# Kernel optimization log

Hardware: AMD Instinct MI355X
Metric: run time of the kernel (lower is better)

The kernel has to match this reference:

```python
import jax, jax.numpy as jnp
import numpy as np

EMBED_DIM = 1024
NUM_HEADS = 16
HEAD_DIM = EMBED_DIM // NUM_HEADS


def setup_inputs() -> dict:
    key = jax.random.key(0)
    ks = jax.random.split(key, 9)
    B, S, D = 2, 2048, EMBED_DIM
    scale = 1.0 / np.sqrt(D)
    x = jax.random.normal(ks[0], (B, S, D), dtype=jnp.float32)
    Wq = jax.random.normal(ks[1], (D, D), dtype=jnp.float32) * scale
    Wk = jax.random.normal(ks[2], (D, D), dtype=jnp.float32) * scale
    Wv = jax.random.normal(ks[3], (D, D), dtype=jnp.float32) * scale
    Wo = jax.random.normal(ks[4], (D, D), dtype=jnp.float32) * scale
    bq = jnp.zeros((D,), jnp.float32)
    bk = jnp.zeros((D,), jnp.float32)
    bv = jnp.zeros((D,), jnp.float32)
    bo = jnp.zeros((D,), jnp.float32)
    return {"x": x, "Wq": Wq, "bq": bq, "Wk": Wk, "bk": bk,
            "Wv": Wv, "bv": bv, "Wo": Wo, "bo": bo}


def reference(x, Wq, bq, Wk, bk, Wv, bv, Wo, bo):
    B, S, D = x.shape
    H, Dh = NUM_HEADS, HEAD_DIM
    # QKV projections -> [B, H, S, Dh]
    q = (x @ Wq + bq).reshape(B, S, H, Dh).transpose(0, 2, 1, 3)
    k = (x @ Wk + bk).reshape(B, S, H, Dh).transpose(0, 2, 1, 3)
    v = (x @ Wv + bv).reshape(B, S, H, Dh).transpose(0, 2, 1, 3)
    # scores [B, H, S, S], scaled by sqrt(head_dim)
    scores = jnp.einsum('bhqd,bhkd->bhqk', q, k) / jnp.sqrt(jnp.float32(Dh))
    attn = jax.nn.softmax(scores, axis=-1)
    out = jnp.einsum('bhqk,bhkd->bhqd', attn, v)  # [B, H, S, Dh]
    out = out.transpose(0, 2, 1, 3).reshape(B, S, D)
    return out @ Wo + bo
```

## Files before the change

kernel.cpp:

```cpp
#include <hip/hip_runtime.h>
#include <hip/hip_bf16.h>

typedef short bf16x8 __attribute__((ext_vector_type(8)));
typedef float f32x4 __attribute__((ext_vector_type(4)));
typedef unsigned uint2v __attribute__((ext_vector_type(2)));

#define MFMA16(a, b, c) __builtin_amdgcn_mfma_f32_16x16x32_bf16((a), (b), (c), 0, 0, 0)

#if __has_builtin(__builtin_amdgcn_exp2f)
#define EXP2(x) __builtin_amdgcn_exp2f(x)
#else
#define EXP2(x) exp2f(x)
#endif

static constexpr int B_ = 2, S_ = 2048, D_ = 1024, H_ = 16, DH = 64;
static constexpr int M_ = B_ * S_;
static constexpr int K_ = D_;
static constexpr float kQS = 0.18033688011112042f;

static __device__ __forceinline__ ushort f2bf(float f) {
    __hip_bfloat16 h = __float2bfloat16(f);
    return *reinterpret_cast<ushort*>(&h);
}
static __device__ __forceinline__ float bf2f(ushort u) {
    __hip_bfloat16 h;
    *reinterpret_cast<ushort*>(&h) = u;
    return __bfloat162float(h);
}

static __device__ __forceinline__ void gload16(const ushort* g, ushort* l) {
    __builtin_amdgcn_global_load_lds((const __attribute__((address_space(1))) void*)g,
                                     (__attribute__((address_space(3))) void*)l, 16, 0, 0);
}

static __device__ __forceinline__ unsigned pkbf(float lo, float hi) {
    return __builtin_amdgcn_perm(__builtin_bit_cast(unsigned, hi),
                                 __builtin_bit_cast(unsigned, lo), 0x07060302u);
}

__global__ __launch_bounds__(256) void prep5(const float* __restrict__ x,
                                             const float* __restrict__ W0,
                                             const float* __restrict__ W1,
                                             const float* __restrict__ W2,
                                             const float* __restrict__ W3,
                                             ushort* __restrict__ xb,
                                             ushort* __restrict__ T0,
                                             ushort* __restrict__ T1,
                                             ushort* __restrict__ T2,
                                             ushort* __restrict__ T3) {
    int z = blockIdx.z;
    int tx = threadIdx.x, ty = threadIdx.y;
    int t = ty * 32 + tx;
    if (z == 4) {
        int blk = blockIdx.y * 32 + blockIdx.x;
#pragma unroll
        for (int k = 0; k < 4; k++) {
            int i = blk * 1024 + k * 256 + t;
            float4 v = reinterpret_cast<const float4*>(x)[i];
            ushort4 o;
            o.x = f2bf(v.x); o.y = f2bf(v.y); o.z = f2bf(v.z); o.w = f2bf(v.w);
            reinterpret_cast<ushort4*>(xb)[i] = o;
        }
        return;
    }
    __shared__ float tile[32][33];
    const float* W = (z == 0) ? W0 : (z == 1) ? W1 : (z == 2) ? W2 : W3;
    ushort* T = (z == 0) ? T0 : (z == 1) ? T1 : (z == 2) ? T2 : T3;
    float sc = (z == 0) ? kQS : 1.0f;
    int bx = blockIdx.x, by = blockIdx.y;
#pragma unroll
    for (int i = 0; i < 4; i++)
        tile[ty + i * 8][tx] = W[(by * 32 + ty + i * 8) * D_ + bx * 32 + tx];
    __syncthreads();
#pragma unroll
    for (int i = 0; i < 4; i++)
        T[(bx * 32 + ty + i * 8) * K_ + by * 32 + tx] = f2bf(tile[tx][ty + i * 8] * sc);
}

template <int MODE, int TN>
__global__ __launch_bounds__(256, 3) void gemm128(const ushort* __restrict__ A,
                                                  const ushort* __restrict__ Wt,
                                                  const float* __restrict__ bias_q,
                                                  const float* __restrict__ bias_k,
                                                  const float* __restrict__ bias_v,
                                                  ushort* __restrict__ Qb,
                                                  ushort* __restrict__ Kb,
                                                  ushort* __restrict__ Vtb,
                                                  float* __restrict__ outf) {
    constexpr int NJ = TN / 32;
    __shared__ __align__(16) ushort As[128 * 32];
    __shared__ __align__(16) ushort Bs[TN * 32];

    int m0 = blockIdx.x * 128;
    int n0 = blockIdx.y * TN;
    int t = threadIdx.x;
    int lane = t & 63, w = t >> 6;
    int ln = lane & 15, lq = lane >> 4;
    int wm = (w >> 1) * 64, wn = (w & 1) * (TN / 2);

    int c0 = t, c1 = t + 256;
    const ushort* Ag0 = A + (size_t)(m0 + (c0 >> 2)) * K_ + (c0 & 3) * 8;
    const ushort* Ag1 = A + (size_t)(m0 + (c1 >> 2)) * K_ + (c1 & 3) * 8;
    const ushort* Bg0 = Wt + (size_t)(n0 + (c0 >> 2)) * K_ + (c0 & 3) * 8;
    const ushort* Bg1 = Wt + (size_t)(n0 + (c1 >> 2)) * K_ + (c1 & 3) * 8;
    ushort* Al0 = As + c0 * 8;
    ushort* Al1 = As + c1 * 8;
    ushort* Bl0 = Bs + c0 * 8;
    ushort* Bl1 = Bs + c1 * 8;

    const bool swp = (MODE == 1) || (n0 < 2048);

    f32x4 acc[4][NJ];
#pragma unroll
    for (int i = 0; i < 4; i++)
#pragma unroll
        for (int j = 0; j < NJ; j++) acc[i][j] = f32x4{0.f, 0.f, 0.f, 0.f};

    if (swp) {
        for (int k0 = 0; k0 < K_; k0 += 32) {
            gload16(Ag0 + k0, Al0);
            gload16(Ag1 + k0, Al1);
            gload16(Bg0 + k0, Bl0);
            if (TN == 128) gload16(Bg1 + k0, Bl1);
            __syncthreads();
            bf16x8 af[4], bfr[NJ];
#pragma unroll
            for (int i = 0; i < 4; i++)
                af[i] = *reinterpret_cast<const bf16x8*>(As + (wm + i * 16 + ln) * 32 + lq * 8);
#pragma unroll
            for (int j = 0; j < NJ; j++)
                bfr[j] = *reinterpret_cast<const bf16x8*>(Bs + (wn + j * 16 + ln) * 32 + lq * 8);
#pragma unroll
            for (int i = 0; i < 4; i++)
#pragma unroll
                for (int j = 0; j < NJ; j++)
                    acc[i][j] = MFMA16(bfr[j], af[i], acc[i][j]);
            __syncthreads();
        }
    } else {
        for (int k0 = 0; k0 < K_; k0 += 32) {
            gload16(Ag0 + k0, Al0);
            gload16(Ag1 + k0, Al1);
            gload16(Bg0 + k0, Bl0);
            if (TN == 128) gload16(Bg1 + k0, Bl1);
            __syncthreads();
            bf16x8 af[4], bfr[NJ];
#pragma unroll
            for (int i = 0; i < 4; i++)
                af[i] = *reinterpret_cast<const bf16x8*>(As + (wm + i * 16 + ln) * 32 + lq * 8);
#pragma unroll
            for (int j = 0; j < NJ; j++)
                bfr[j] = *reinterpret_cast<const bf16x8*>(Bs + (wn + j * 16 + ln) * 32 + lq * 8);
#pragma unroll
            for (int i = 0; i < 4; i++)
#pragma unroll
                for (int j = 0; j < NJ; j++)
                    acc[i][j] = MFMA16(af[i], bfr[j], acc[i][j]);
            __syncthreads();
        }
    }

    if (MODE == 1) {
#pragma unroll
        for (int j = 0; j < NJ; j++) {
            int nb = n0 + wn + j * 16 + lq * 4;
            float4 bv4 = *reinterpret_cast<const float4*>(bias_q + nb);
#pragma unroll
            for (int i = 0; i < 4; i++) {
                int m = m0 + wm + i * 16 + ln;
                float4 o;
                o.x = acc[i][j][0] + bv4.x;
                o.y = acc[i][j][1] + bv4.y;
                o.z = acc[i][j][2] + bv4.z;
                o.w = acc[i][j][3] + bv4.w;
                *reinterpret_cast<float4*>(outf + (size_t)m * D_ + nb) = o;
            }
        }
    } else if (n0 < 2048) {
        int which = n0 >> 10;
        const float* bp = which ? bias_k : bias_q;
        ushort* dst = which ? Kb : Qb;
        float bsc = which ? 1.0f : kQS;
#pragma unroll
        for (int j = 0; j < NJ; j++) {
            int nb = ((n0 + wn + j * 16) & 1023) + lq * 4;
            int h = nb >> 6, dhb = nb & 63;
            float4 bv4 = *reinterpret_cast<const float4*>(bp + nb);
            bv4.x *= bsc; bv4.y *= bsc; bv4.z *= bsc; bv4.w *= bsc;
#pragma unroll
            for (int i = 0; i < 4; i++) {
                int m = m0 + wm + i * 16 + ln;
                int b = m >> 11, s = m & 2047;
                ushort4 o4;
                o4.x = f2bf(acc[i][j][0] + bv4.x);
                o4.y = f2bf(acc[i][j][1] + bv4.y);
                o4.z = f2bf(acc[i][j][2] + bv4.z);
                o4.w = f2bf(acc[i][j][3] + bv4.w);
                *reinterpret_cast<ushort4*>(dst + (((size_t)(b * H_ + h) * S_) + s) * DH + dhb) = o4;
            }
        }
    } else {
#pragma unroll
        for (int j = 0; j < NJ; j++) {
            int n = n0 + wn + j * 16 + ln;
            int nn = n & 1023, h = nn >> 6, dh = nn & 63;
            float bv = bias_v[nn];
#pragma unroll
            for (int i = 0; i < 4; i++) {
                int m = m0 + wm + i * 16 + lq * 4;
                int b = m >> 11, s0 = m & 2047;
                ushort4 o4;
                o4.x = f2bf(acc[i][j][0] + bv);
                o4.y = f2bf(acc[i][j][1] + bv);
                o4.z = f2bf(acc[i][j][2] + bv);
                o4.w = f2bf(acc[i][j][3] + bv);
                *reinterpret_cast<ushort4*>(Vtb + (((size_t)(b * H_ + h) * DH) + dh) * S_ + s0) = o4;
            }
        }
    }
}

__global__ __launch_bounds__(256, 4) void gemm64(const ushort* __restrict__ A,
                                                 const ushort* __restrict__ Wt,
                                                 const float* __restrict__ bias,
                                                 float* __restrict__ outf) {
    __shared__ __align__(16) ushort As[64 * 32];
    __shared__ __align__(16) ushort Bs[64 * 32];

    int m0 = blockIdx.x * 64;
    int n0 = blockIdx.y * 64;
    int t = threadIdx.x;
    int lane = t & 63, w = t >> 6;
    int ln = lane & 15, lq = lane >> 4;
    int wm = (w >> 1) * 32, wn = (w & 1) * 32;

    int c0 = t;
    const ushort* Ag0 = A + (size_t)(m0 + (c0 >> 2)) * K_ + (c0 & 3) * 8;
    const ushort* Bg0 = Wt + (size_t)(n0 + (c0 >> 2)) * K_ + (c0 & 3) * 8;
    ushort* Al0 = As + c0 * 8;
    ushort* Bl0 = Bs + c0 * 8;

    f32x4 acc[2][2];
#pragma unroll
    for (int i = 0; i < 2; i++)
#pragma unroll
        for (int j = 0; j < 2; j++) acc[i][j] = f32x4{0.f, 0.f, 0.f, 0.f};

    for (int k0 = 0; k0 < K_; k0 += 32) {
        gload16(Ag0 + k0, Al0);
        gload16(Bg0 + k0, Bl0);
        __syncthreads();
        bf16x8 af[2], bfr[2];
#pragma unroll
        for (int i = 0; i < 2; i++)
            af[i] = *reinterpret_cast<const bf16x8*>(As + (wm + i * 16 + ln) * 32 + lq * 8);
#pragma unroll
        for (int j = 0; j < 2; j++)
            bfr[j] = *reinterpret_cast<const bf16x8*>(Bs + (wn + j * 16 + ln) * 32 + lq * 8);
#pragma unroll
        for (int i = 0; i < 2; i++)
#pragma unroll
            for (int j = 0; j < 2; j++)
                acc[i][j] = MFMA16(bfr[j], af[i], acc[i][j]);
        __syncthreads();
    }

#pragma unroll
    for (int j = 0; j < 2; j++) {
        int nb = n0 + wn + j * 16 + lq * 4;
        float4 bv4 = *reinterpret_cast<const float4*>(bias + nb);
#pragma unroll
        for (int i = 0; i < 2; i++) {
            int m = m0 + wm + i * 16 + ln;
            float4 o;
            o.x = acc[i][j][0] + bv4.x;
            o.y = acc[i][j][1] + bv4.y;
            o.z = acc[i][j][2] + bv4.z;
            o.w = acc[i][j][3] + bv4.w;
            *reinterpret_cast<float4*>(outf + (size_t)m * D_ + nb) = o;
        }
    }
}

__global__ __launch_bounds__(256, 4) void attn128s(const ushort* __restrict__ Q,
                                                   const ushort* __restrict__ K,
                                                   const ushort* __restrict__ Vt,
                                                   ushort* __restrict__ O1,
                                                   ushort* __restrict__ O2,
                                                   float* __restrict__ L) {
    __shared__ __align__(16) ushort Kl[512 * 8];
    __shared__ __align__(16) ushort Vl[512 * 8];
    __shared__ __align__(16) ushort Pl[4][2][16 * 72];

    int bid = blockIdx.x;
    int half = bid >> 9;
    int rem = bid & 511;
    int qb = rem & 15;
    int bh = rem >> 4;
    int t = threadIdx.x;
    int lane = t & 63, w = t >> 6;
    int ln = lane & 15, lq = lane >> 4;
    int q0 = qb * 128 + w * 32;

    const ushort* Qp = Q + (size_t)bh * S_ * DH;
    const ushort* Kp = K + (size_t)bh * S_ * DH + (size_t)half * 1024 * DH;
    const ushort* Vp = Vt + (size_t)bh * DH * S_ + (size_t)half * 1024;

    bf16x8 qf[2][2];
#pragma unroll
    for (int tl = 0; tl < 2; tl++) {
        const ushort* qp = Qp + (q0 + tl * 16 + ln) * DH + lq * 8;
        qf[tl][0] = *reinterpret_cast<const bf16x8*>(qp);
        qf[tl][1] = *reinterpret_cast<const bf16x8*>(qp + 32);
    }

    bf16x8 ones;
#pragma unroll
    for (int j = 0; j < 8; j++) ones[j] = (short)0x3F80;

    int c0 = t, c1 = t + 256;
    const ushort* Kg0 = Kp + (size_t)(c0 & 63) * DH + (c0 >> 6) * 8;
    const ushort* Kg1 = Kp + (size_t)(c1 & 63) * DH + (c1 >> 6) * 8;
    const ushort* Vg0 = Vp + (size_t)(c0 & 63) * S_ + (c0 >> 6) * 8;
    const ushort* Vg1 = Vp + (size_t)(c1 & 63) * S_ + (c1 >> 6) * 8;
    ushort* Kl0 = Kl + c0 * 8;
    ushort* Kl1 = Kl + c1 * 8;
    ushort* Vl0 = Vl + c0 * 8;
    ushort* Vl1 = Vl + c1 * 8;

    f32x4 o_acc[2][4];
    f32x4 l_acc[2];
#pragma unroll
    for (int tl = 0; tl < 2; tl++) {
        l_acc[tl] = f32x4{0.f, 0.f, 0.f, 0.f};
#pragma unroll
        for (int nt = 0; nt < 4; nt++) o_acc[tl][nt] = f32x4{0.f, 0.f, 0.f, 0.f};
    }

    for (int kt = 0; kt < 16; kt++) {
        int kb = kt * 64;
        gload16(Kg0 + (size_t)kb * DH, Kl0);
        gload16(Kg1 + (size_t)kb * DH, Kl1);
        gload16(Vg0 + kb, Vl0);
        gload16(Vg1 + kb, Vl1);
        __syncthreads();

        f32x4 sc[2][4];
#pragma unroll
        for (int nt = 0; nt < 4; nt++) {
            bf16x8 kf0 = *reinterpret_cast<const bf16x8*>(Kl + (lq * 64 + nt * 16 + ln) * 8);
            bf16x8 kf1 = *reinterpret_cast<const bf16x8*>(Kl + ((4 + lq) * 64 + nt * 16 + ln) * 8);
#pragma unroll
            for (int tl = 0; tl < 2; tl++) {
                f32x4 c = {0.f, 0.f, 0.f, 0.f};
                c = MFMA16(kf0, qf[tl][0], c);
                c = MFMA16(kf1, qf[tl][1], c);
                sc[tl][nt] = c;
            }
        }
#pragma unroll
        for (int tl = 0; tl < 2; tl++)
#pragma unroll
            for (int nt = 0; nt < 4; nt++) {
                float p0 = EXP2(sc[tl][nt][0]);
                float p1 = EXP2(sc[tl][nt][1]);
                float p2 = EXP2(sc[tl][nt][2]);
                float p3 = EXP2(sc[tl][nt][3]);
                uint2v pk;
                pk.x = pkbf(p0, p1);
                pk.y = pkbf(p2, p3);
                *reinterpret_cast<uint2v*>(&Pl[w][tl][ln * 72 + nt * 16 + lq * 4]) = pk;
            }
        bf16x8 pf[2][2];
#pragma unroll
        for (int tl = 0; tl < 2; tl++) {
            pf[tl][0] = *reinterpret_cast<const bf16x8*>(&Pl[w][tl][ln * 72 + lq * 8]);
            pf[tl][1] = *reinterpret_cast<const bf16x8*>(&Pl[w][tl][ln * 72 + 32 + lq * 8]);
            l_acc[tl] = MFMA16(pf[tl][0], ones, l_acc[tl]);
            l_acc[tl] = MFMA16(pf[tl][1], ones, l_acc[tl]);
        }
#pragma unroll
        for (int nt = 0; nt < 4; nt++) {
            bf16x8 vf0 = *reinterpret_cast<const bf16x8*>(Vl + (lq * 64 + nt * 16 + ln) * 8);
            bf16x8 vf1 = *reinterpret_cast<const bf16x8*>(Vl + ((4 + lq) * 64 + nt * 16 + ln) * 8);
#pragma unroll
            for (int tl = 0; tl < 2; tl++) {
                o_acc[tl][nt] = MFMA16(pf[tl][0], vf0, o_acc[tl][nt]);
                o_acc[tl][nt] = MFMA16(pf[tl][1], vf1, o_acc[tl][nt]);
            }
        }
        __syncthreads();
    }

    ushort* Op = half ? O2 : O1;
    float* Lp = L + ((size_t)half * 32 + bh) * S_;
    int b = bh >> 4, h = bh & 15;
#pragma unroll
    for (int tl = 0; tl < 2; tl++) {
        float linv[4];
#pragma unroll
        for (int r = 0; r < 4; r++) {
            linv[r] = 1.0f / l_acc[tl][r];
            if (ln == 0) Lp[q0 + tl * 16 + lq * 4 + r] = l_acc[tl][r];
        }
#pragma unroll
        for (int nt = 0; nt < 4; nt++)
#pragma unroll
            for (int r = 0; r < 4; r++) {
                int s = q0 + tl * 16 + lq * 4 + r;
                Op[((b * S_ + s) * H_ + h) * DH + nt * 16 + ln] =
                    f2bf(o_acc[tl][nt][r] * linv[r]);
            }
    }
}

__global__ __launch_bounds__(256) void attn_comb(const ushort* __restrict__ O1,
                                                 const ushort* __restrict__ O2,
                                                 const float* __restrict__ L,
                                                 ushort* __restrict__ AO) {
    int i = blockIdx.x * 256 + threadIdx.x;
    int row = i >> 7;
    int col = (i & 127) * 8;
    int h = col >> 6;
    int b = row >> 11, s = row & 2047;
    int bh = b * 16 + h;
    float l1 = L[(size_t)bh * S_ + s];
    float l2 = L[((size_t)32 + bh) * S_ + s];
    float inv = 1.0f / (l1 + l2);
    float w1 = l1 * inv, w2 = l2 * inv;
    size_t off = (size_t)row * D_ + col;
    ushort4 a0 = reinterpret_cast<const ushort4*>(O1 + off)[0];
    ushort4 a1 = reinterpret_cast<const ushort4*>(O1 + off)[1];
    ushort4 b0 = reinterpret_cast<const ushort4*>(O2 + off)[0];
    ushort4 b1 = reinterpret_cast<const ushort4*>(O2 + off)[1];
    ushort4 o0, o1v;
    o0.x = f2bf(w1 * bf2f(a0.x) + w2 * bf2f(b0.x));
    o0.y = f2bf(w1 * bf2f(a0.y) + w2 * bf2f(b0.y));
    o0.z = f2bf(w1 * bf2f(a0.z) + w2 * bf2f(b0.z));
    o0.w = f2bf(w1 * bf2f(a0.w) + w2 * bf2f(b0.w));
    o1v.x = f2bf(w1 * bf2f(a1.x) + w2 * bf2f(b1.x));
    o1v.y = f2bf(w1 * bf2f(a1.y) + w2 * bf2f(b1.y));
    o1v.z = f2bf(w1 * bf2f(a1.z) + w2 * bf2f(b1.z));
    o1v.w = f2bf(w1 * bf2f(a1.w) + w2 * bf2f(b1.w));
    reinterpret_cast<ushort4*>(AO + off)[0] = o0;
    reinterpret_cast<ushort4*>(AO + off)[1] = o1v;
}

extern "C" void kernel_launch(void* const* d_in, const int* in_sizes, int n_in,
                              void* d_out, int out_size, void* d_ws, size_t ws_size,
                              hipStream_t stream) {
    const float* x  = (const float*)d_in[0];
    const float* Wq = (const float*)d_in[1];
    const float* bq = (const float*)d_in[2];
    const float* Wk = (const float*)d_in[3];
    const float* bk = (const float*)d_in[4];
    const float* Wv = (const float*)d_in[5];
    const float* bv = (const float*)d_in[6];
    const float* Wo = (const float*)d_in[7];
    const float* bo = (const float*)d_in[8];
    float* out = (float*)d_out;

    char* ws = (char*)d_ws;
    const size_t MB = 1024 * 1024;
    ushort* wtq = (ushort*)(ws + 0 * MB);
    ushort* wtk = (ushort*)(ws + 2 * MB);
    ushort* wtv = (ushort*)(ws + 4 * MB);
    ushort* wto = (ushort*)(ws + 6 * MB);
    ushort* xb  = (ushort*)(ws + 8 * MB);
    ushort* Qb  = (ushort*)(ws + 16 * MB);
    ushort* Kb  = (ushort*)(ws + 24 * MB);
    ushort* Vtb = (ushort*)(ws + 32 * MB);
    ushort* AO  = (ushort*)(ws + 40 * MB);
    ushort* O1  = (ushort*)(ws + 8 * MB);
    ushort* O2  = (ushort*)(ws + 48 * MB);
    float*  Lw  = (float*)(ws + 56 * MB);

    prep5<<<dim3(32, 32, 5), dim3(32, 8), 0, stream>>>(
        x, Wq, Wk, Wv, Wo, xb, wtq, wtk, wtv, wto);

    gemm128<0, 128><<<dim3(M_ / 128, 3072 / 128), 256, 0, stream>>>(
        xb, wtq, bq, bk, bv, Qb, Kb, Vtb, nullptr);

    attn128s<<<1024, 256, 0, stream>>>(Qb, Kb, Vtb, O1, O2, Lw);
    attn_comb<<<(M_ * D_ / 8) / 256, 256, 0, stream>>>(O1, O2, Lw, AO);

    gemm64<<<dim3(M_ / 64, D_ / 64), 256, 0, stream>>>(AO, wto, bo, out);
}
```

Baseline: 196.3 us.

## Fuse split-attention combine into output projection GEMM prologue with double-buffered B

Removes the separate attn_comb kernel and its AO round-trip through global memory. The output-projection GEMM now loads both partial attention outputs and their L weights, combines them in registers, and writes the A tile to shared memory. The W tile is double-buffered with a register prefetch of the next A inputs. In exchange, the combine work is repeated for every N-block (16 times), so O1/O2 reads and the combine arithmetic are multiplied, and A loads go through registers instead of async direct loads.

```diff
diff --git a/kernel.cpp b/kernel.cpp
--- a/kernel.cpp
+++ b/kernel.cpp
@@ -4,6 +4,7 @@
 typedef short bf16x8 __attribute__((ext_vector_type(8)));
 typedef float f32x4 __attribute__((ext_vector_type(4)));
 typedef unsigned uint2v __attribute__((ext_vector_type(2)));
+typedef unsigned uint4v __attribute__((ext_vector_type(4)));
 
 #define MFMA16(a, b, c) __builtin_amdgcn_mfma_f32_16x16x32_bf16((a), (b), (c), 0, 0, 0)
 
@@ -220,12 +221,14 @@
     }
 }
 
-__global__ __launch_bounds__(256, 4) void gemm64(const ushort* __restrict__ A,
-                                                 const ushort* __restrict__ Wt,
-                                                 const float* __restrict__ bias,
-                                                 float* __restrict__ outf) {
+__global__ __launch_bounds__(256, 4) void gemm64c(const ushort* __restrict__ O1,
+                                                  const ushort* __restrict__ O2,
+                                                  const float* __restrict__ L,
+                                                  const ushort* __restrict__ Wt,
+                                                  const float* __restrict__ bias,
+                                                  float* __restrict__ outf) {
     __shared__ __align__(16) ushort As[64 * 32];
-    __shared__ __align__(16) ushort Bs[64 * 32];
+    __shared__ __align__(16) ushort Bs[2][64 * 32];
 
     int m0 = blockIdx.x * 64;
     int n0 = blockIdx.y * 64;
@@ -234,11 +237,15 @@
     int ln = lane & 15, lq = lane >> 4;
     int wm = (w >> 1) * 32, wn = (w & 1) * 32;
 
-    int c0 = t;
-    const ushort* Ag0 = A + (size_t)(m0 + (c0 >> 2)) * K_ + (c0 & 3) * 8;
-    const ushort* Bg0 = Wt + (size_t)(n0 + (c0 >> 2)) * K_ + (c0 & 3) * 8;
-    ushort* Al0 = As + c0 * 8;
-    ushort* Bl0 = Bs + c0 * 8;
+    int m = m0 + (t >> 2);
+    int b = m >> 11, s = m & 2047;
+    const ushort* O1g = O1 + (size_t)m * D_ + (t & 3) * 8;
+    const ushort* O2g = O2 + (size_t)m * D_ + (t & 3) * 8;
+    const float* L1p = L + (size_t)(b * 16) * S_ + s;
+    const float* L2p = L + (size_t)(32 + b * 16) * S_ + s;
+    ushort* Alw = As + t * 8;
+    const ushort* Bg0 = Wt + (size_t)(n0 + (t >> 2)) * K_ + (t & 3) * 8;
+    ushort* Bl = Bs[0] + t * 8;
 
     f32x4 acc[2][2];
 #pragma unroll
@@ -246,23 +253,49 @@
 #pragma unroll
         for (int j = 0; j < 2; j++) acc[i][j] = f32x4{0.f, 0.f, 0.f, 0.f};
 
-    for (int k0 = 0; k0 < K_; k0 += 32) {
-        gload16(Ag0 + k0, Al0);
-        gload16(Bg0 + k0, Bl0);
+    uint4v o1r = *reinterpret_cast<const uint4v*>(O1g);
+    uint4v o2r = *reinterpret_cast<const uint4v*>(O2g);
+    float l1 = L1p[0];
+    float l2 = L2p[0];
+    gload16(Bg0, Bs[0] + t * 8);
+
+    for (int kt = 0; kt < 32; kt++) {
+        int cur = kt & 1;
         __syncthreads();
+        {
+            float inv = 1.0f / (l1 + l2);
+            float w1 = l1 * inv, w2 = l2 * inv;
+            const ushort* a1 = reinterpret_cast<const ushort*>(&o1r);
+            const ushort* a2 = reinterpret_cast<const ushort*>(&o2r);
+            ushort cmb[8];
+#pragma unroll
+            for (int e = 0; e < 8; e++)
+                cmb[e] = f2bf(w1 * bf2f(a1[e]) + w2 * bf2f(a2[e]));
+            *reinterpret_cast<uint4v*>(Alw) = *reinterpret_cast<const uint4v*>(cmb);
+        }
+        __syncthreads();
+        if (kt < 31) {
+            int k0n = (kt + 1) * 32;
+            o1r = *reinterpret_cast<const uint4v*>(O1g + k0n);
+            o2r = *reinterpret_cast<const uint4v*>(O2g + k0n);
+            int hn = k0n >> 6;
+            l1 = L1p[(size_t)hn * S_];
+            l2 = L2p[(size_t)hn * S_];
+            gload16(Bg0 + k0n, Bs[cur ^ 1] + t * 8);
+        }
+        const ushort* Bsc = Bs[cur];
         bf16x8 af[2], bfr[2];
 #pragma unroll
         for (int i = 0; i < 2; i++)
             af[i] = *reinterpret_cast<const bf16x8*>(As + (wm + i * 16 + ln) * 32 + lq * 8);
 #pragma unroll
         for (int j = 0; j < 2; j++)
-            bfr[j] = *reinterpret_cast<const bf16x8*>(Bs + (wn + j * 16 + ln) * 32 + lq * 8);
+            bfr[j] = *reinterpret_cast<const bf16x8*>(Bsc + (wn + j * 16 + ln) * 32 + lq * 8);
 #pragma unroll
         for (int i = 0; i < 2; i++)
 #pragma unroll
             for (int j = 0; j < 2; j++)
                 acc[i][j] = MFMA16(bfr[j], af[i], acc[i][j]);
-        __syncthreads();
     }
 
 #pragma unroll
@@ -271,13 +304,13 @@
         float4 bv4 = *reinterpret_cast<const float4*>(bias + nb);
 #pragma unroll
         for (int i = 0; i < 2; i++) {
-            int m = m0 + wm + i * 16 + ln;
+            int mm = m0 + wm + i * 16 + ln;
             float4 o;
             o.x = acc[i][j][0] + bv4.x;
             o.y = acc[i][j][1] + bv4.y;
             o.z = acc[i][j][2] + bv4.z;
             o.w = acc[i][j][3] + bv4.w;
-            *reinterpret_cast<float4*>(outf + (size_t)m * D_ + nb) = o;
+            *reinterpret_cast<float4*>(outf + (size_t)mm * D_ + nb) = o;
         }
     }
 }
@@ -412,38 +445,6 @@
                     f2bf(o_acc[tl][nt][r] * linv[r]);
             }
     }
-}
-
-__global__ __launch_bounds__(256) void attn_comb(const ushort* __restrict__ O1,
-                                                 const ushort* __restrict__ O2,
-                                                 const float* __restrict__ L,
-                                                 ushort* __restrict__ AO) {
-    int i = blockIdx.x * 256 + threadIdx.x;
-    int row = i >> 7;
-    int col = (i & 127) * 8;
-    int h = col >> 6;
-    int b = row >> 11, s = row & 2047;
-    int bh = b * 16 + h;
-    float l1 = L[(size_t)bh * S_ + s];
-    float l2 = L[((size_t)32 + bh) * S_ + s];
-    float inv = 1.0f / (l1 + l2);
-    float w1 = l1 * inv, w2 = l2 * inv;
-    size_t off = (size_t)row * D_ + col;
-    ushort4 a0 = reinterpret_cast<const ushort4*>(O1 + off)[0];
-    ushort4 a1 = reinterpret_cast<const ushort4*>(O1 + off)[1];
-    ushort4 b0 = reinterpret_cast<const ushort4*>(O2 + off)[0];
-    ushort4 b1 = reinterpret_cast<const ushort4*>(O2 + off)[1];
-    ushort4 o0, o1v;
-    o0.x = f2bf(w1 * bf2f(a0.x) + w2 * bf2f(b0.x));
-    o0.y = f2bf(w1 * bf2f(a0.y) + w2 * bf2f(b0.y));
-    o0.z = f2bf(w1 * bf2f(a0.z) + w2 * bf2f(b0.z));
-    o0.w = f2bf(w1 * bf2f(a0.w) + w2 * bf2f(b0.w));
-    o1v.x = f2bf(w1 * bf2f(a1.x) + w2 * bf2f(b1.x));
-    o1v.y = f2bf(w1 * bf2f(a1.y) + w2 * bf2f(b1.y));
-    o1v.z = f2bf(w1 * bf2f(a1.z) + w2 * bf2f(b1.z));
-    o1v.w = f2bf(w1 * bf2f(a1.w) + w2 * bf2f(b1.w));
-    reinterpret_cast<ushort4*>(AO + off)[0] = o0;
-    reinterpret_cast<ushort4*>(AO + off)[1] = o1v;
 }
 
 extern "C" void kernel_launch(void* const* d_in, const int* in_sizes, int n_in,
@@ -470,7 +471,6 @@
     ushort* Qb  = (ushort*)(ws + 16 * MB);
     ushort* Kb  = (ushort*)(ws + 24 * MB);
     ushort* Vtb = (ushort*)(ws + 32 * MB);
-    ushort* AO  = (ushort*)(ws + 40 * MB);
     ushort* O1  = (ushort*)(ws + 8 * MB);
     ushort* O2  = (ushort*)(ws + 48 * MB);
     float*  Lw  = (float*)(ws + 56 * MB);
@@ -482,7 +482,6 @@
         xb, wtq, bq, bk, bv, Qb, Kb, Vtb, nullptr);
 
     attn128s<<<1024, 256, 0, stream>>>(Qb, Kb, Vtb, O1, O2, Lw);
-    attn_comb<<<(M_ * D_ / 8) / 256, 256, 0, stream>>>(O1, O2, Lw, AO);
-
-    gemm64<<<dim3(M_ / 64, D_ / 64), 256, 0, stream>>>(AO, wto, bo, out);
-}
+
+    gemm64c<<<dim3(M_ / 64, D_ / 64), 256, 0, stream>>>(O1, O2, Lw, wto, bo, out);
+}
```

After: 200.5 us. 2.1% more time.
